# Kernel tuning notes

Measured on AMD Instinct MI355X. Metric: run time of the kernel, lower is better.

The kernel has to match this reference:

```python
import jax, jax.numpy as jnp
import numpy as np

N_NODES = 100000
N_EDGES = 3200000
IN_DIM, HID_DIM, OUT_DIM = 256, 128, 64


def setup_inputs() -> dict:
    key = jax.random.key(0)
    ks = jax.random.split(key, 8)
    x = jax.random.normal(ks[0], (N_NODES, IN_DIM), dtype=jnp.float32)
    edge_index = jax.random.randint(ks[1], (2, N_EDGES), 0, N_NODES, dtype=jnp.int64)
    s = 0.05
    return {
        "x": x,
        "edge_index": edge_index,
        "W1": jax.random.normal(ks[2], (IN_DIM, HID_DIM), dtype=jnp.float32) * s,
        "b1": jnp.zeros((HID_DIM,), dtype=jnp.float32),
        "W2": jax.random.normal(ks[3], (HID_DIM, HID_DIM), dtype=jnp.float32) * s,
        "b2": jnp.zeros((HID_DIM,), dtype=jnp.float32),
        "W3": jax.random.normal(ks[4], (HID_DIM, OUT_DIM), dtype=jnp.float32) * s,
        "b3": jnp.zeros((OUT_DIM,), dtype=jnp.float32),
    }


def _gcn_conv(x, src, dst, deg_inv_sqrt, W, b):
    """PyG GCNConv: D^-1/2 (A+I) D^-1/2 (X W) + b.
    src/dst already include self-loops; deg_inv_sqrt precomputed per node."""
    h = x @ W  # [N, F_out] - transform first (smaller message dim)
    norm = deg_inv_sqrt[src] * deg_inv_sqrt[dst]  # [E]
    msg = h[src] * norm[:, None]  # gather + scale
    out = jax.ops.segment_sum(msg, dst, num_segments=x.shape[0])  # scatter-add
    return out + b


def reference(x, edge_index, W1, b1, W2, b2, W3, b3):
    n = x.shape[0]
    loops = jnp.arange(n, dtype=edge_index.dtype)
    src = jnp.concatenate([edge_index[0], loops])
    dst = jnp.concatenate([edge_index[1], loops])
    # symmetric normalization degree over (A + I), counted on dst as in PyG
    deg = jax.ops.segment_sum(jnp.ones_like(dst, dtype=x.dtype), dst, num_segments=n)
    deg_inv_sqrt = jnp.where(deg > 0, jax.lax.rsqrt(deg), 0.0)

    h = _gcn_conv(x, src, dst, deg_inv_sqrt, W1, b1)
    h = jax.nn.relu(h)  # dropout in eval mode = identity
    h = _gcn_conv(h, src, dst, deg_inv_sqrt, W2, b2)
    h = jax.nn.relu(h)
    h = _gcn_conv(h, src, dst, deg_inv_sqrt, W3, b3)
    return h
```

## Files before the change

kernel.cpp:

```cpp
#include <hip/hip_runtime.h>
#include <hip/hip_fp16.h>

constexpr int IN_DIM  = 256;
constexpr int HID_DIM = 128;
constexpr int OUT_DIM = 64;

constexpr int NPB_SHIFT = 8;
constexpr int NPB   = 1 << NPB_SHIFT;
constexpr int NBMAX = 512;
constexpr int CHUNK = 4096;
constexpr int CAP_B = 12288;

typedef _Float16 half8 __attribute__((ext_vector_type(8)));
typedef float floatx4 __attribute__((ext_vector_type(4)));


__global__ __launch_bounds__(256) void k_hist(const int* __restrict__ dst, int E, int NB,
                                              int* __restrict__ bsize) {
  __shared__ int h[NBMAX];
  for (int i = threadIdx.x; i < NB; i += 256) h[i] = 0;
  __syncthreads();
  int e0 = blockIdx.x * CHUNK;
  int e1 = min(e0 + CHUNK, E);
  for (int e = e0 + threadIdx.x; e < e1; e += 256) {
    int d = __builtin_nontemporal_load(&dst[e]);
    atomicAdd(&h[d >> NPB_SHIFT], 1);
  }
  __syncthreads();
  for (int b = threadIdx.x; b < NB; b += 256) {
    int c = h[b];
    if (c) atomicAdd(&bsize[b], c);
  }
}

__global__ __launch_bounds__(512) void k_scanb(const int* __restrict__ bsize, int NB, int E,
                                               int* __restrict__ boff, int* __restrict__ gcur) {
  __shared__ int sh[NBMAX + 1];
  for (int i = threadIdx.x; i < NB; i += 512) sh[i] = bsize[i];
  __syncthreads();
  if (threadIdx.x == 0) {
    int run = 0;
    for (int b = 0; b < NB; b++) { int v = sh[b]; sh[b] = run; run += v; }
    sh[NB] = run;
  }
  __syncthreads();
  for (int i = threadIdx.x; i < NB; i += 512) { boff[i] = sh[i]; gcur[i] = sh[i]; }
  if (threadIdx.x == 0) boff[NB] = sh[NB];
}

__global__ __launch_bounds__(256) void k_binA(const int* __restrict__ src,
                                              const int* __restrict__ dst, int E, int NB,
                                              int* __restrict__ gcur,
                                              unsigned int* __restrict__ bin) {
  __shared__ unsigned int sbuf[CHUNK];
  __shared__ unsigned short sbb[CHUNK];
  __shared__ int h[NBMAX], lofs[NBMAX], wofs[NBMAX], hcur[NBMAX];
  for (int i = threadIdx.x; i < NB; i += 256) h[i] = 0;
  __syncthreads();
  int e0 = blockIdx.x * CHUNK;
  int e1 = min(e0 + CHUNK, E);
  for (int e = e0 + threadIdx.x; e < e1; e += 256) {
    int d = __builtin_nontemporal_load(&dst[e]);
    atomicAdd(&h[d >> NPB_SHIFT], 1);
  }
  __syncthreads();
  for (int b = threadIdx.x; b < NB; b += 256) {
    int c = h[b];
    if (c) wofs[b] = atomicAdd(&gcur[b], c);
  }
  if (threadIdx.x == 0) {
    int run = 0;
    for (int b = 0; b < NB; b++) { lofs[b] = run; run += h[b]; }
  }
  __syncthreads();
  for (int b = threadIdx.x; b < NB; b += 256) hcur[b] = lofs[b];
  __syncthreads();
  for (int e = e0 + threadIdx.x; e < e1; e += 256) {
    int d = dst[e];
    int s = src[e];
    int b = d >> NPB_SHIFT;
    int p = atomicAdd(&hcur[b], 1);
    sbuf[p] = ((unsigned int)(d & (NPB - 1)) << 24) | (unsigned int)s;
    sbb[p] = (unsigned short)b;
  }
  __syncthreads();
  int total = e1 - e0;
  for (int i = threadIdx.x; i < total; i += 256) {
    int b = sbb[i];
    bin[(size_t)wofs[b] + (i - lofs[b])] = sbuf[i];
  }
}

__global__ __launch_bounds__(256) void k_passB(const unsigned int* __restrict__ bin,
                                               const int* __restrict__ boff, int NB, int N, int E,
                                               int* __restrict__ rowptr, float* __restrict__ dis,
                                               int* __restrict__ col) {
  __shared__ unsigned int colbuf[CAP_B];
  __shared__ int lcnt[NPB], lofs2[NPB + 1], lpos[NPB];
  int b = blockIdx.x;
  int lo = b << NPB_SHIFT;
  int e0 = boff[b], e1 = boff[b + 1];
  int tot = e1 - e0;
  if (threadIdx.x < NPB) lcnt[threadIdx.x] = 0;
  __syncthreads();
  for (int i = threadIdx.x; i < tot; i += 256) {
    unsigned int v = bin[(size_t)e0 + i];
    atomicAdd(&lcnt[v >> 24], 1);
  }
  __syncthreads();
  if (threadIdx.x == 0) {
    int run = 0;
    for (int i = 0; i < NPB; i++) { lofs2[i] = run; run += lcnt[i]; }
    lofs2[NPB] = run;
  }
  __syncthreads();
  if (threadIdx.x < NPB) {
    int node = lo + threadIdx.x;
    if (node < N) {
      rowptr[node] = e0 + lofs2[threadIdx.x];
      dis[node] = rsqrtf((float)lcnt[threadIdx.x] + 1.0f);
    }
    lpos[threadIdx.x] = lofs2[threadIdx.x];
  }
  __syncthreads();
  for (int i = threadIdx.x; i < tot; i += 256) {
    unsigned int v = bin[(size_t)e0 + i];
    int idx = v >> 24;
    int p = atomicAdd(&lpos[idx], 1);
    unsigned int s = v & 0x00FFFFFFu;
    if (p < CAP_B) colbuf[p] = s;
    else col[(size_t)e0 + p] = (int)s;
  }
  __syncthreads();
  int cp = min(tot, CAP_B);
  for (int i = threadIdx.x; i < cp; i += 256)
    __builtin_nontemporal_store(colbuf[i], (unsigned int*)&col[(size_t)e0 + i]);
  if (b == 0 && threadIdx.x == 0) rowptr[N] = E;
}


template <int K, int N>
__device__ inline void packW_one(const float* __restrict__ W, _Float16* __restrict__ Wp,
                                 int idx) {
  int k = idx / N, n = idx % N;
  int ct = n >> 4, ks = k >> 5, q = (k >> 3) & 3, j = k & 7;
  int lane = (n & 15) + (q << 4);
  Wp[((((size_t)ct * (K / 32) + ks) * 64 + lane) << 3) + j] = (_Float16)W[idx];
}

__global__ __launch_bounds__(256) void k_packAll(const float* __restrict__ W1, _Float16* __restrict__ Wp1,
                                                 const float* __restrict__ W2, _Float16* __restrict__ Wp2,
                                                 const float* __restrict__ W3, _Float16* __restrict__ Wp3) {
  constexpr int S1 = IN_DIM * HID_DIM;
  constexpr int S2 = S1 + HID_DIM * HID_DIM;
  constexpr int S3 = S2 + HID_DIM * OUT_DIM;
  int idx = blockIdx.x * 256 + threadIdx.x;
  if (idx < S1) packW_one<IN_DIM, HID_DIM>(W1, Wp1, idx);
  else if (idx < S2) packW_one<HID_DIM, HID_DIM>(W2, Wp2, idx - S1);
  else if (idx < S3) packW_one<HID_DIM, OUT_DIM>(W3, Wp3, idx - S2);
}


template <int K, int N, typename AT>
__global__ __launch_bounds__(256) void k_gemm_mfma(const AT* __restrict__ A,
                                                   const _Float16* __restrict__ Wp,
                                                   const float* __restrict__ dis,
                                                   __half* __restrict__ out, int M) {
  constexpr int CT = N / 16;
  constexpr int KS = K / 32;
  constexpr int KH = (K * N * 2 > 32768) ? 2 : 1;
  constexpr int KSH = KS / KH;
  constexpr int NF4 = CT * KSH * 64;
  __shared__ float4 wlds[NF4];

  const int wave = threadIdx.x >> 6, lane = threadIdx.x & 63;
  const int q = lane >> 4, mlane = lane & 15;
  const int row0 = blockIdx.x * 64 + wave * 16;
  int arow = row0 + mlane;
  if (arow > M - 1) arow = M - 1;

  const float4* __restrict__ wsrc = (const float4*)Wp;

  floatx4 acc[CT];
#pragma unroll
  for (int c = 0; c < CT; c++) acc[c] = (floatx4){0.f, 0.f, 0.f, 0.f};

#pragma unroll
  for (int h = 0; h < KH; h++) {
    if (h) __syncthreads();
#pragma unroll
    for (int i = threadIdx.x; i < NF4; i += 256) {
      int c = i / (KSH * 64);
      int rem = i & (KSH * 64 - 1);
      wlds[i] = wsrc[(size_t)(c * KS + h * KSH) * 64 + rem];
    }
    __syncthreads();

#pragma unroll
    for (int ksl = 0; ksl < KSH; ksl++) {
      const int ks = h * KSH + ksl;
      half8 a;
      if constexpr (sizeof(AT) == 4) {
        const float* ap = &A[(size_t)arow * K + ks * 32 + q * 8];
        float4 f0 = *(const float4*)ap;
        float4 f1 = *(const float4*)(ap + 4);
        a[0] = (_Float16)f0.x; a[1] = (_Float16)f0.y;
        a[2] = (_Float16)f0.z; a[3] = (_Float16)f0.w;
        a[4] = (_Float16)f1.x; a[5] = (_Float16)f1.y;
        a[6] = (_Float16)f1.z; a[7] = (_Float16)f1.w;
      } else {
        a = *(const half8*)&A[(size_t)arow * K + ks * 32 + q * 8];
      }
#pragma unroll
      for (int c = 0; c < CT; c++) {
        half8 b = *(const half8*)&wlds[(c * KSH + ksl) * 64 + lane];
        acc[c] = __builtin_amdgcn_mfma_f32_16x16x32_f16(a, b, acc[c], 0, 0, 0);
      }
    }
  }

  float dv[4]; int orow[4];
#pragma unroll
  for (int r = 0; r < 4; r++) {
    orow[r] = row0 + q * 4 + r;
    dv[r] = (orow[r] < M) ? dis[orow[r]] : 0.f;
  }
#pragma unroll
  for (int c = 0; c < CT; c++) {
    int cl = c * 16 + mlane;
#pragma unroll
    for (int r = 0; r < 4; r++)
      if (orow[r] < M)
        out[(size_t)orow[r] * N + cl] = __float2half_rn(dv[r] * acc[c][r]);
  }
}


template <bool RELU>
__global__ __launch_bounds__(256) void k_agg128(const __half* __restrict__ g,
                                                const int* __restrict__ rowptr,
                                                const int* __restrict__ col,
                                                const float* __restrict__ dis,
                                                const float* __restrict__ bias,
                                                __half* __restrict__ out, int n, int v0) {
  const int lane = threadIdx.x & 63;
  const int r = lane >> 4;
  const int c = lane & 15;
  const int v = v0 + blockIdx.x * 4 + (threadIdx.x >> 6);
  if (v >= n) return;
  int p = rowptr[v], end = rowptr[v + 1];
  const float dv = dis[v];

  float acc[8];
#pragma unroll
  for (int i = 0; i < 8; i++) acc[i] = 0.f;
  if (r == 0) {
    half8 s = *(const half8*)&g[(size_t)v * 128 + c * 8];
#pragma unroll
    for (int i = 0; i < 8; i++) acc[i] += (float)s[i];
  }

  while (p < end) {
    int navail = end - p;
    if (navail > 64) navail = 64;
    int cv = __builtin_nontemporal_load(&col[p + (lane < navail ? lane : 0)]);
    int done = 0;
    while (navail - done >= 8) {
      int u0 = __shfl(cv, done + r);
      int u1 = __shfl(cv, done + 4 + r);
      half8 t0 = *(const half8*)&g[(size_t)u0 * 128 + c * 8];
      half8 t1 = *(const half8*)&g[(size_t)u1 * 128 + c * 8];
#pragma unroll
      for (int i = 0; i < 8; i++) acc[i] += (float)t0[i];
#pragma unroll
      for (int i = 0; i < 8; i++) acc[i] += (float)t1[i];
      done += 8;
    }
    int remn = navail - done;
    if (remn > 0) {
      int m0 = remn < 4 ? remn : 4;
      int u0 = __shfl(cv, done + (r < m0 ? r : 0));
      half8 t0 = *(const half8*)&g[(size_t)u0 * 128 + c * 8];
      float k0 = (r < m0) ? 1.f : 0.f;
#pragma unroll
      for (int i = 0; i < 8; i++) acc[i] = fmaf(k0, (float)t0[i], acc[i]);
      if (remn > 4) {
        int m1 = remn - 4;
        int u1 = __shfl(cv, done + 4 + (r < m1 ? r : 0));
        half8 t1 = *(const half8*)&g[(size_t)u1 * 128 + c * 8];
        float k1 = (r < m1) ? 1.f : 0.f;
#pragma unroll
        for (int i = 0; i < 8; i++) acc[i] = fmaf(k1, (float)t1[i], acc[i]);
      }
    }
    p += navail;
  }

#pragma unroll
  for (int i = 0; i < 8; i++) {
    acc[i] += __shfl_xor(acc[i], 16);
    acc[i] += __shfl_xor(acc[i], 32);
  }

  if (r == 0) {
    half8 h;
#pragma unroll
    for (int i = 0; i < 8; i++) {
      float o = fmaf(dv, acc[i], bias[c * 8 + i]);
      if (RELU) o = fmaxf(o, 0.f);
      h[i] = (_Float16)o;
    }
    *(half8*)&out[(size_t)v * 128 + c * 8] = h;
  }
}


__global__ __launch_bounds__(256) void k_agg64(const __half* __restrict__ g,
                                               const int* __restrict__ rowptr,
                                               const int* __restrict__ col,
                                               const float* __restrict__ dis,
                                               const float* __restrict__ bias,
                                               float* __restrict__ out, int n) {
  const int lane = threadIdx.x & 63;
  const int r = lane >> 3;
  const int c = lane & 7;
  const int v = blockIdx.x * 4 + (threadIdx.x >> 6);
  if (v >= n) return;
  int p = rowptr[v], end = rowptr[v + 1];
  const float dv = dis[v];

  float acc[8];
#pragma unroll
  for (int i = 0; i < 8; i++) acc[i] = 0.f;
  if (r == 0) {
    half8 s = *(const half8*)&g[(size_t)v * 64 + c * 8];
#pragma unroll
    for (int i = 0; i < 8; i++) acc[i] += (float)s[i];
  }

  while (p < end) {
    int navail = end - p;
    if (navail > 64) navail = 64;
    int cv = __builtin_nontemporal_load(&col[p + (lane < navail ? lane : 0)]);
    int done = 0;
    while (navail - done >= 16) {
      int u0 = __shfl(cv, done + r);
      int u1 = __shfl(cv, done + 8 + r);
      half8 t0 = *(const half8*)&g[(size_t)u0 * 64 + c * 8];
      half8 t1 = *(const half8*)&g[(size_t)u1 * 64 + c * 8];
#pragma unroll
      for (int i = 0; i < 8; i++) acc[i] += (float)t0[i];
#pragma unroll
      for (int i = 0; i < 8; i++) acc[i] += (float)t1[i];
      done += 16;
    }
    int remn = navail - done;
    if (remn > 0) {
      int m0 = remn < 8 ? remn : 8;
      int u0 = __shfl(cv, done + (r < m0 ? r : 0));
      half8 t0 = *(const half8*)&g[(size_t)u0 * 64 + c * 8];
      float k0 = (r < m0) ? 1.f : 0.f;
#pragma unroll
      for (int i = 0; i < 8; i++) acc[i] = fmaf(k0, (float)t0[i], acc[i]);
      if (remn > 8) {
        int m1 = remn - 8;
        int u1 = __shfl(cv, done + 8 + (r < m1 ? r : 0));
        half8 t1 = *(const half8*)&g[(size_t)u1 * 64 + c * 8];
        float k1 = (r < m1) ? 1.f : 0.f;
#pragma unroll
        for (int i = 0; i < 8; i++) acc[i] = fmaf(k1, (float)t1[i], acc[i]);
      }
    }
    p += navail;
  }

#pragma unroll
  for (int i = 0; i < 8; i++) {
    acc[i] += __shfl_xor(acc[i], 8);
    acc[i] += __shfl_xor(acc[i], 16);
    acc[i] += __shfl_xor(acc[i], 32);
  }

  if (r == 0) {
    float4 o0, o1;
    float ov[8];
#pragma unroll
    for (int i = 0; i < 8; i++) ov[i] = fmaf(dv, acc[i], bias[c * 8 + i]);
    o0.x = ov[0]; o0.y = ov[1]; o0.z = ov[2]; o0.w = ov[3];
    o1.x = ov[4]; o1.y = ov[5]; o1.z = ov[6]; o1.w = ov[7];
    *(float4*)&out[(size_t)v * 64 + c * 8]     = o0;
    *(float4*)&out[(size_t)v * 64 + c * 8 + 4] = o1;
  }
}


extern "C" void kernel_launch(void* const* d_in, const int* in_sizes, int n_in,
                              void* d_out, int out_size, void* d_ws, size_t ws_size,
                              hipStream_t stream) {
  const float* x  = (const float*)d_in[0];
  const int*   ei = (const int*)d_in[1];
  const float* W1 = (const float*)d_in[2];
  const float* b1 = (const float*)d_in[3];
  const float* W2 = (const float*)d_in[4];
  const float* b2 = (const float*)d_in[5];
  const float* W3 = (const float*)d_in[6];
  const float* b3 = (const float*)d_in[7];
  float* outp = (float*)d_out;

  const int N = in_sizes[0] / IN_DIM;
  const int E = in_sizes[1] / 2;
  const int* src = ei;
  const int* dst = ei + E;
  const int NB = (N + NPB - 1) >> NPB_SHIFT;

  char* w = (char*)d_ws;
  auto take = [&](size_t bytes) {
    char* r = w;
    w += (bytes + 255) & ~size_t(255);
    return r;
  };
  float*  dis    = (float*)take((size_t)N * 4);
  int*    rowptr = (int*)take((size_t)(N + 1) * 4);
  int*    bsize  = (int*)take((size_t)NB * 4);
  int*    boff   = (int*)take((size_t)(NB + 1) * 4);
  int*    gcur   = (int*)take((size_t)NB * 4);
  int*    col    = (int*)take((size_t)E * 4);
  unsigned int* bin = (unsigned int*)take((size_t)E * 4);
  _Float16* Wp1  = (_Float16*)take((size_t)IN_DIM * HID_DIM * 2);
  _Float16* Wp2  = (_Float16*)take((size_t)HID_DIM * HID_DIM * 2);
  _Float16* Wp3  = (_Float16*)take((size_t)HID_DIM * OUT_DIM * 2);
  __half* gbuf   = (__half*)take((size_t)N * 128 * 2);
  __half* bufH   = (__half*)take((size_t)N * 128 * 2);

  const int cb = (E + CHUNK - 1) / CHUNK;
  hipMemsetAsync(bsize, 0, (size_t)NB * 4, stream);
  hipLaunchKernelGGL(k_hist, dim3(cb), dim3(256), 0, stream, dst, E, NB, bsize);
  hipLaunchKernelGGL(k_scanb, dim3(1), dim3(512), 0, stream, bsize, NB, E, boff, gcur);
  hipLaunchKernelGGL(k_binA, dim3(cb), dim3(256), 0, stream, src, dst, E, NB, gcur, bin);
  hipLaunchKernelGGL(k_passB, dim3(NB), dim3(256), 0, stream, bin, boff, NB, N, E, rowptr, dis, col);

  hipLaunchKernelGGL(k_packAll, dim3((IN_DIM * HID_DIM + HID_DIM * HID_DIM + HID_DIM * OUT_DIM + 255) / 256),
                     dim3(256), 0, stream, W1, Wp1, W2, Wp2, W3, Wp3);

  const int gb = (N + 63) / 64;
  const int ab = (N + 3) / 4;
  const int nh = (N + 1) / 2;
  const int ab1 = (nh + 3) / 4;
  const int ab2 = (N - nh + 3) / 4;
  hipLaunchKernelGGL((k_gemm_mfma<IN_DIM, HID_DIM, float>), dim3(gb), dim3(256), 0, stream, x, Wp1, dis, gbuf, N);
  hipLaunchKernelGGL((k_agg128<true>), dim3(ab1), dim3(256), 0, stream, gbuf, rowptr, col, dis, b1, bufH, N, 0);
  hipLaunchKernelGGL((k_agg128<true>), dim3(ab2), dim3(256), 0, stream, gbuf, rowptr, col, dis, b1, bufH, N, nh);
  hipLaunchKernelGGL((k_gemm_mfma<HID_DIM, HID_DIM, __half>), dim3(gb), dim3(256), 0, stream, bufH, Wp2, dis, gbuf, N);
  hipLaunchKernelGGL((k_agg128<true>), dim3(ab1), dim3(256), 0, stream, gbuf, rowptr, col, dis, b2, bufH, N, 0);
  hipLaunchKernelGGL((k_agg128<true>), dim3(ab2), dim3(256), 0, stream, gbuf, rowptr, col, dis, b2, bufH, N, nh);
  hipLaunchKernelGGL((k_gemm_mfma<HID_DIM, OUT_DIM, __half>), dim3(gb), dim3(256), 0, stream, bufH, Wp3, dis, gbuf, N);
  hipLaunchKernelGGL(k_agg64, dim3(ab), dim3(256), 0, stream, gbuf, rowptr, col, dis, b3, outp, N);
}
```

Measured before the change: 595.3 us.

## Make GEMM persistent with whole-weight LDS staging and 512-thread blocks

The feature-transform GEMM now loads the full packed weight matrix into LDS once per block and loops over 128-row tiles in a persistent grid capped at 512 blocks, using 512-thread blocks. Before, every 64-row block reloaded the weights, in two halves for the first layer. The aim is to cut the repeated weight traffic and block launch overhead. For K=256, N=128 the LDS footprint grows to 64 KB per block, which limits occupancy, and the persistent loop may hide less global-load latency.

Result: slower. 736.6 us (+23.7%).

```diff
diff --git a/kernel.cpp b/kernel.cpp
--- a/kernel.cpp
+++ b/kernel.cpp
@@ -162,43 +162,34 @@
 
 
 template <int K, int N, typename AT>
-__global__ __launch_bounds__(256) void k_gemm_mfma(const AT* __restrict__ A,
-                                                   const _Float16* __restrict__ Wp,
-                                                   const float* __restrict__ dis,
-                                                   __half* __restrict__ out, int M) {
+__global__ __launch_bounds__(512, 4) void k_gemm_mfma(const AT* __restrict__ A,
+                                                      const _Float16* __restrict__ Wp,
+                                                      const float* __restrict__ dis,
+                                                      __half* __restrict__ out, int M,
+                                                      int ntiles) {
   constexpr int CT = N / 16;
   constexpr int KS = K / 32;
-  constexpr int KH = (K * N * 2 > 32768) ? 2 : 1;
-  constexpr int KSH = KS / KH;
-  constexpr int NF4 = CT * KSH * 64;
+  constexpr int NF4 = CT * KS * 64;
   __shared__ float4 wlds[NF4];
 
   const int wave = threadIdx.x >> 6, lane = threadIdx.x & 63;
   const int q = lane >> 4, mlane = lane & 15;
-  const int row0 = blockIdx.x * 64 + wave * 16;
-  int arow = row0 + mlane;
-  if (arow > M - 1) arow = M - 1;
-
-  const float4* __restrict__ wsrc = (const float4*)Wp;
-
-  floatx4 acc[CT];
-#pragma unroll
-  for (int c = 0; c < CT; c++) acc[c] = (floatx4){0.f, 0.f, 0.f, 0.f};
-
-#pragma unroll
-  for (int h = 0; h < KH; h++) {
-    if (h) __syncthreads();
-#pragma unroll
-    for (int i = threadIdx.x; i < NF4; i += 256) {
-      int c = i / (KSH * 64);
-      int rem = i & (KSH * 64 - 1);
-      wlds[i] = wsrc[(size_t)(c * KS + h * KSH) * 64 + rem];
-    }
-    __syncthreads();
-
-#pragma unroll
-    for (int ksl = 0; ksl < KSH; ksl++) {
-      const int ks = h * KSH + ksl;
+
+  for (int i = threadIdx.x; i < NF4; i += 512)
+    wlds[i] = ((const float4*)Wp)[i];
+  __syncthreads();
+
+  for (int t = blockIdx.x; t < ntiles; t += gridDim.x) {
+    const int row0 = t * 128 + wave * 16;
+    int arow = row0 + mlane;
+    if (arow > M - 1) arow = M - 1;
+
+    floatx4 acc[CT];
+#pragma unroll
+    for (int c = 0; c < CT; c++) acc[c] = (floatx4){0.f, 0.f, 0.f, 0.f};
+
+#pragma unroll
+    for (int ks = 0; ks < KS; ks++) {
       half8 a;
       if constexpr (sizeof(AT) == 4) {
         const float* ap = &A[(size_t)arow * K + ks * 32 + q * 8];
@@ -213,25 +204,25 @@
       }
 #pragma unroll
       for (int c = 0; c < CT; c++) {
-        half8 b = *(const half8*)&wlds[(c * KSH + ksl) * 64 + lane];
+        half8 b = *(const half8*)&wlds[(c * KS + ks) * 64 + lane];
         acc[c] = __builtin_amdgcn_mfma_f32_16x16x32_f16(a, b, acc[c], 0, 0, 0);
       }
     }
-  }
-
-  float dv[4]; int orow[4];
-#pragma unroll
-  for (int r = 0; r < 4; r++) {
-    orow[r] = row0 + q * 4 + r;
-    dv[r] = (orow[r] < M) ? dis[orow[r]] : 0.f;
-  }
-#pragma unroll
-  for (int c = 0; c < CT; c++) {
-    int cl = c * 16 + mlane;
-#pragma unroll
-    for (int r = 0; r < 4; r++)
-      if (orow[r] < M)
-        out[(size_t)orow[r] * N + cl] = __float2half_rn(dv[r] * acc[c][r]);
+
+    float dv[4]; int orow[4];
+#pragma unroll
+    for (int r = 0; r < 4; r++) {
+      orow[r] = row0 + q * 4 + r;
+      dv[r] = (orow[r] < M) ? dis[orow[r]] : 0.f;
+    }
+#pragma unroll
+    for (int c = 0; c < CT; c++) {
+      int cl = c * 16 + mlane;
+#pragma unroll
+      for (int r = 0; r < 4; r++)
+        if (orow[r] < M)
+          out[(size_t)orow[r] * N + cl] = __float2half_rn(dv[r] * acc[c][r]);
+    }
   }
 }
 
@@ -442,17 +433,18 @@
   hipLaunchKernelGGL(k_packAll, dim3((IN_DIM * HID_DIM + HID_DIM * HID_DIM + HID_DIM * OUT_DIM + 255) / 256),
                      dim3(256), 0, stream, W1, Wp1, W2, Wp2, W3, Wp3);
 
-  const int gb = (N + 63) / 64;
+  const int ntiles = (N + 127) / 128;
+  const int ggrid = ntiles < 512 ? ntiles : 512;
   const int ab = (N + 3) / 4;
   const int nh = (N + 1) / 2;
   const int ab1 = (nh + 3) / 4;
   const int ab2 = (N - nh + 3) / 4;
-  hipLaunchKernelGGL((k_gemm_mfma<IN_DIM, HID_DIM, float>), dim3(gb), dim3(256), 0, stream, x, Wp1, dis, gbuf, N);
+  hipLaunchKernelGGL((k_gemm_mfma<IN_DIM, HID_DIM, float>), dim3(ggrid), dim3(512), 0, stream, x, Wp1, dis, gbuf, N, ntiles);
   hipLaunchKernelGGL((k_agg128<true>), dim3(ab1), dim3(256), 0, stream, gbuf, rowptr, col, dis, b1, bufH, N, 0);
   hipLaunchKernelGGL((k_agg128<true>), dim3(ab2), dim3(256), 0, stream, gbuf, rowptr, col, dis, b1, bufH, N, nh);
-  hipLaunchKernelGGL((k_gemm_mfma<HID_DIM, HID_DIM, __half>), dim3(gb), dim3(256), 0, stream, bufH, Wp2, dis, gbuf, N);
+  hipLaunchKernelGGL((k_gemm_mfma<HID_DIM, HID_DIM, __half>), dim3(ggrid), dim3(512), 0, stream, bufH, Wp2, dis, gbuf, N, ntiles);
   hipLaunchKernelGGL((k_agg128<true>), dim3(ab1), dim3(256), 0, stream, gbuf, rowptr, col, dis, b2, bufH, N, 0);
   hipLaunchKernelGGL((k_agg128<true>), dim3(ab2), dim3(256), 0, stream, gbuf, rowptr, col, dis, b2, bufH, N, nh);
-  hipLaunchKernelGGL((k_gemm_mfma<HID_DIM, OUT_DIM, __half>), dim3(gb), dim3(256), 0, stream, bufH, Wp3, dis, gbuf, N);
+  hipLaunchKernelGGL((k_gemm_mfma<HID_DIM, OUT_DIM, __half>), dim3(ggrid), dim3(512), 0, stream, bufH, Wp3, dis, gbuf, N, ntiles);
   hipLaunchKernelGGL(k_agg64, dim3(ab), dim3(256), 0, stream, gbuf, rowptr, col, dis, b3, outp, N);
 }
```

## Replace two-pass bucketed CSR build with atomic degree count and scatter

Applied to the files above, without the earlier changes.

Replaces the histogram/scan/bin/local-sort CSR construction with a simpler scheme: per-node degree atomics, a wave-level scan with an atomic global offset to allocate each row's segment, and a direct atomic-cursor scatter of source indices. Aggregation kernels now read row start plus degree instead of a contiguous rowptr. This removes several kernels and the intermediate bin buffer, but rows are no longer laid out in node order and neighbour order within a row is nondeterministic. The scattered 3.2M global atomics and random writes may cost more than the locality-friendly bucketed approach, and row allocation order can hurt col locality in aggregation.

After: 917.4 us. 1.54x slower.

```diff
diff --git a/kernel.cpp b/kernel.cpp
--- a/kernel.cpp
+++ b/kernel.cpp
@@ -5,137 +5,55 @@
 constexpr int HID_DIM = 128;
 constexpr int OUT_DIM = 64;
 
-constexpr int NPB_SHIFT = 8;
-constexpr int NPB   = 1 << NPB_SHIFT;
-constexpr int NBMAX = 512;
-constexpr int CHUNK = 4096;
-constexpr int CAP_B = 12288;
-
 typedef _Float16 half8 __attribute__((ext_vector_type(8)));
 typedef float floatx4 __attribute__((ext_vector_type(4)));
 
 
-__global__ __launch_bounds__(256) void k_hist(const int* __restrict__ dst, int E, int NB,
-                                              int* __restrict__ bsize) {
-  __shared__ int h[NBMAX];
-  for (int i = threadIdx.x; i < NB; i += 256) h[i] = 0;
-  __syncthreads();
-  int e0 = blockIdx.x * CHUNK;
-  int e1 = min(e0 + CHUNK, E);
-  for (int e = e0 + threadIdx.x; e < e1; e += 256) {
+__global__ __launch_bounds__(256) void k_deg(const int* __restrict__ dst, int E,
+                                             int* __restrict__ deg) {
+  const int stride = gridDim.x * 256;
+  for (int e = blockIdx.x * 256 + threadIdx.x; e < E; e += stride) {
     int d = __builtin_nontemporal_load(&dst[e]);
-    atomicAdd(&h[d >> NPB_SHIFT], 1);
-  }
-  __syncthreads();
-  for (int b = threadIdx.x; b < NB; b += 256) {
-    int c = h[b];
-    if (c) atomicAdd(&bsize[b], c);
-  }
-}
-
-__global__ __launch_bounds__(512) void k_scanb(const int* __restrict__ bsize, int NB, int E,
-                                               int* __restrict__ boff, int* __restrict__ gcur) {
-  __shared__ int sh[NBMAX + 1];
-  for (int i = threadIdx.x; i < NB; i += 512) sh[i] = bsize[i];
-  __syncthreads();
-  if (threadIdx.x == 0) {
-    int run = 0;
-    for (int b = 0; b < NB; b++) { int v = sh[b]; sh[b] = run; run += v; }
-    sh[NB] = run;
-  }
-  __syncthreads();
-  for (int i = threadIdx.x; i < NB; i += 512) { boff[i] = sh[i]; gcur[i] = sh[i]; }
-  if (threadIdx.x == 0) boff[NB] = sh[NB];
-}
-
-__global__ __launch_bounds__(256) void k_binA(const int* __restrict__ src,
-                                              const int* __restrict__ dst, int E, int NB,
-                                              int* __restrict__ gcur,
-                                              unsigned int* __restrict__ bin) {
-  __shared__ unsigned int sbuf[CHUNK];
-  __shared__ unsigned short sbb[CHUNK];
-  __shared__ int h[NBMAX], lofs[NBMAX], wofs[NBMAX], hcur[NBMAX];
-  for (int i = threadIdx.x; i < NB; i += 256) h[i] = 0;
-  __syncthreads();
-  int e0 = blockIdx.x * CHUNK;
-  int e1 = min(e0 + CHUNK, E);
-  for (int e = e0 + threadIdx.x; e < e1; e += 256) {
+    atomicAdd(&deg[d], 1);
+  }
+}
+
+__global__ __launch_bounds__(256) void k_alloc(const int* __restrict__ deg, int N,
+                                               int* __restrict__ tot,
+                                               int* __restrict__ rowbeg,
+                                               int* __restrict__ cur,
+                                               float* __restrict__ dis) {
+  const int v = blockIdx.x * 256 + threadIdx.x;
+  const int lane = threadIdx.x & 63;
+  int d = (v < N) ? deg[v] : 0;
+  int inc = d;
+#pragma unroll
+  for (int off = 1; off < 64; off <<= 1) {
+    int t = __shfl_up(inc, off);
+    if (lane >= off) inc += t;
+  }
+  int wtot = __shfl(inc, 63);
+  int base = 0;
+  if (lane == 63) base = atomicAdd(tot, wtot);
+  base = __shfl(base, 63) + (inc - d);
+  if (v < N) {
+    rowbeg[v] = base;
+    cur[v] = base;
+    dis[v] = rsqrtf((float)d + 1.0f);
+  }
+}
+
+__global__ __launch_bounds__(256) void k_scat(const int* __restrict__ src,
+                                              const int* __restrict__ dst, int E,
+                                              int* __restrict__ cur,
+                                              int* __restrict__ col) {
+  const int stride = gridDim.x * 256;
+  for (int e = blockIdx.x * 256 + threadIdx.x; e < E; e += stride) {
     int d = __builtin_nontemporal_load(&dst[e]);
-    atomicAdd(&h[d >> NPB_SHIFT], 1);
-  }
-  __syncthreads();
-  for (int b = threadIdx.x; b < NB; b += 256) {
-    int c = h[b];
-    if (c) wofs[b] = atomicAdd(&gcur[b], c);
-  }
-  if (threadIdx.x == 0) {
-    int run = 0;
-    for (int b = 0; b < NB; b++) { lofs[b] = run; run += h[b]; }
-  }
-  __syncthreads();
-  for (int b = threadIdx.x; b < NB; b += 256) hcur[b] = lofs[b];
-  __syncthreads();
-  for (int e = e0 + threadIdx.x; e < e1; e += 256) {
-    int d = dst[e];
-    int s = src[e];
-    int b = d >> NPB_SHIFT;
-    int p = atomicAdd(&hcur[b], 1);
-    sbuf[p] = ((unsigned int)(d & (NPB - 1)) << 24) | (unsigned int)s;
-    sbb[p] = (unsigned short)b;
-  }
-  __syncthreads();
-  int total = e1 - e0;
-  for (int i = threadIdx.x; i < total; i += 256) {
-    int b = sbb[i];
-    bin[(size_t)wofs[b] + (i - lofs[b])] = sbuf[i];
-  }
-}
-
-__global__ __launch_bounds__(256) void k_passB(const unsigned int* __restrict__ bin,
-                                               const int* __restrict__ boff, int NB, int N, int E,
-                                               int* __restrict__ rowptr, float* __restrict__ dis,
-                                               int* __restrict__ col) {
-  __shared__ unsigned int colbuf[CAP_B];
-  __shared__ int lcnt[NPB], lofs2[NPB + 1], lpos[NPB];
-  int b = blockIdx.x;
-  int lo = b << NPB_SHIFT;
-  int e0 = boff[b], e1 = boff[b + 1];
-  int tot = e1 - e0;
-  if (threadIdx.x < NPB) lcnt[threadIdx.x] = 0;
-  __syncthreads();
-  for (int i = threadIdx.x; i < tot; i += 256) {
-    unsigned int v = bin[(size_t)e0 + i];
-    atomicAdd(&lcnt[v >> 24], 1);
-  }
-  __syncthreads();
-  if (threadIdx.x == 0) {
-    int run = 0;
-    for (int i = 0; i < NPB; i++) { lofs2[i] = run; run += lcnt[i]; }
-    lofs2[NPB] = run;
-  }
-  __syncthreads();
-  if (threadIdx.x < NPB) {
-    int node = lo + threadIdx.x;
-    if (node < N) {
-      rowptr[node] = e0 + lofs2[threadIdx.x];
-      dis[node] = rsqrtf((float)lcnt[threadIdx.x] + 1.0f);
-    }
-    lpos[threadIdx.x] = lofs2[threadIdx.x];
-  }
-  __syncthreads();
-  for (int i = threadIdx.x; i < tot; i += 256) {
-    unsigned int v = bin[(size_t)e0 + i];
-    int idx = v >> 24;
-    int p = atomicAdd(&lpos[idx], 1);
-    unsigned int s = v & 0x00FFFFFFu;
-    if (p < CAP_B) colbuf[p] = s;
-    else col[(size_t)e0 + p] = (int)s;
-  }
-  __syncthreads();
-  int cp = min(tot, CAP_B);
-  for (int i = threadIdx.x; i < cp; i += 256)
-    __builtin_nontemporal_store(colbuf[i], (unsigned int*)&col[(size_t)e0 + i]);
-  if (b == 0 && threadIdx.x == 0) rowptr[N] = E;
+    int s = __builtin_nontemporal_load(&src[e]);
+    int p = atomicAdd(&cur[d], 1);
+    col[p] = s;
+  }
 }
 
 
@@ -238,7 +156,8 @@
 
 template <bool RELU>
 __global__ __launch_bounds__(256) void k_agg128(const __half* __restrict__ g,
-                                                const int* __restrict__ rowptr,
+                                                const int* __restrict__ rowbeg,
+                                                const int* __restrict__ deg,
                                                 const int* __restrict__ col,
                                                 const float* __restrict__ dis,
                                                 const float* __restrict__ bias,
@@ -248,7 +167,8 @@
   const int c = lane & 15;
   const int v = v0 + blockIdx.x * 4 + (threadIdx.x >> 6);
   if (v >= n) return;
-  int p = rowptr[v], end = rowptr[v + 1];
+  int p = rowbeg[v];
+  int end = p + deg[v];
   const float dv = dis[v];
 
   float acc[8];
@@ -316,7 +236,8 @@
 
 
 __global__ __launch_bounds__(256) void k_agg64(const __half* __restrict__ g,
-                                               const int* __restrict__ rowptr,
+                                               const int* __restrict__ rowbeg,
+                                               const int* __restrict__ deg,
                                                const int* __restrict__ col,
                                                const float* __restrict__ dis,
                                                const float* __restrict__ bias,
@@ -326,7 +247,8 @@
   const int c = lane & 7;
   const int v = blockIdx.x * 4 + (threadIdx.x >> 6);
   if (v >= n) return;
-  int p = rowptr[v], end = rowptr[v + 1];
+  int p = rowbeg[v];
+  int end = p + deg[v];
   const float dv = dis[v];
 
   float acc[8];
@@ -411,7 +333,6 @@
   const int E = in_sizes[1] / 2;
   const int* src = ei;
   const int* dst = ei + E;
-  const int NB = (N + NPB - 1) >> NPB_SHIFT;
 
   char* w = (char*)d_ws;
   auto take = [&](size_t bytes) {
@@ -420,24 +341,20 @@
     return r;
   };
   float*  dis    = (float*)take((size_t)N * 4);
-  int*    rowptr = (int*)take((size_t)(N + 1) * 4);
-  int*    bsize  = (int*)take((size_t)NB * 4);
-  int*    boff   = (int*)take((size_t)(NB + 1) * 4);
-  int*    gcur   = (int*)take((size_t)NB * 4);
+  int*    rowbeg = (int*)take((size_t)N * 4);
+  int*    cur    = (int*)take((size_t)N * 4);
+  int*    deg    = (int*)take((size_t)(N + 1) * 4);
   int*    col    = (int*)take((size_t)E * 4);
-  unsigned int* bin = (unsigned int*)take((size_t)E * 4);
   _Float16* Wp1  = (_Float16*)take((size_t)IN_DIM * HID_DIM * 2);
   _Float16* Wp2  = (_Float16*)take((size_t)HID_DIM * HID_DIM * 2);
   _Float16* Wp3  = (_Float16*)take((size_t)HID_DIM * OUT_DIM * 2);
   __half* gbuf   = (__half*)take((size_t)N * 128 * 2);
   __half* bufH   = (__half*)take((size_t)N * 128 * 2);
 
-  const int cb = (E + CHUNK - 1) / CHUNK;
-  hipMemsetAsync(bsize, 0, (size_t)NB * 4, stream);
-  hipLaunchKernelGGL(k_hist, dim3(cb), dim3(256), 0, stream, dst, E, NB, bsize);
-  hipLaunchKernelGGL(k_scanb, dim3(1), dim3(512), 0, stream, bsize, NB, E, boff, gcur);
-  hipLaunchKernelGGL(k_binA, dim3(cb), dim3(256), 0, stream, src, dst, E, NB, gcur, bin);
-  hipLaunchKernelGGL(k_passB, dim3(NB), dim3(256), 0, stream, bin, boff, NB, N, E, rowptr, dis, col);
+  hipMemsetAsync(deg, 0, (size_t)(N + 1) * 4, stream);
+  hipLaunchKernelGGL(k_deg, dim3(2048), dim3(256), 0, stream, dst, E, deg);
+  hipLaunchKernelGGL(k_alloc, dim3((N + 255) / 256), dim3(256), 0, stream, deg, N, deg + N, rowbeg, cur, dis);
+  hipLaunchKernelGGL(k_scat, dim3(2048), dim3(256), 0, stream, src, dst, E, cur, col);
 
   hipLaunchKernelGGL(k_packAll, dim3((IN_DIM * HID_DIM + HID_DIM * HID_DIM + HID_DIM * OUT_DIM + 255) / 256),
                      dim3(256), 0, stream, W1, Wp1, W2, Wp2, W3, Wp3);
@@ -448,11 +365,11 @@
   const int ab1 = (nh + 3) / 4;
   const int ab2 = (N - nh + 3) / 4;
   hipLaunchKernelGGL((k_gemm_mfma<IN_DIM, HID_DIM, float>), dim3(gb), dim3(256), 0, stream, x, Wp1, dis, gbuf, N);
-  hipLaunchKernelGGL((k_agg128<true>), dim3(ab1), dim3(256), 0, stream, gbuf, rowptr, col, dis, b1, bufH, N, 0);
-  hipLaunchKernelGGL((k_agg128<true>), dim3(ab2), dim3(256), 0, stream, gbuf, rowptr, col, dis, b1, bufH, N, nh);
+  hipLaunchKernelGGL((k_agg128<true>), dim3(ab1), dim3(256), 0, stream, gbuf, rowbeg, deg, col, dis, b1, bufH, N, 0);
+  hipLaunchKernelGGL((k_agg128<true>), dim3(ab2), dim3(256), 0, stream, gbuf, rowbeg, deg, col, dis, b1, bufH, N, nh);
   hipLaunchKernelGGL((k_gemm_mfma<HID_DIM, HID_DIM, __half>), dim3(gb), dim3(256), 0, stream, bufH, Wp2, dis, gbuf, N);
-  hipLaunchKernelGGL((k_agg128<true>), dim3(ab1), dim3(256), 0, stream, gbuf, rowptr, col, dis, b2, bufH, N, 0);
-  hipLaunchKernelGGL((k_agg128<true>), dim3(ab2), dim3(256), 0, stream, gbuf, rowptr, col, dis, b2, bufH, N, nh);
+  hipLaunchKernelGGL((k_agg128<true>), dim3(ab1), dim3(256), 0, stream, gbuf, rowbeg, deg, col, dis, b2, bufH, N, 0);
+  hipLaunchKernelGGL((k_agg128<true>), dim3(ab2), dim3(256), 0, stream, gbuf, rowbeg, deg, col, dis, b2, bufH, N, nh);
   hipLaunchKernelGGL((k_gemm_mfma<HID_DIM, OUT_DIM, __half>), dim3(gb), dim3(256), 0, stream, bufH, Wp3, dis, gbuf, N);
-  hipLaunchKernelGGL(k_agg64, dim3(ab), dim3(256), 0, stream, gbuf, rowptr, col, dis, b3, outp, N);
-}
+  hipLaunchKernelGGL(k_agg64, dim3(ab), dim3(256), 0, stream, gbuf, rowbeg, deg, col, dis, b3, outp, N);
+}
```
